# Optimization experiments

Measured on AMD Instinct MI355X. Metric: run time of the kernel, lower is better.

Reference implementation:

```python
import jax, jax.numpy as jnp
import numpy as np

EMBED_DIM = 1024
NUM_HEADS = 16
HEAD_DIM = EMBED_DIM // NUM_HEADS
SEQ_LEN = 4096


def setup_inputs() -> dict:
    key = jax.random.key(0)
    kx, kq, kk, kv = jax.random.split(key, 4)
    x = jax.random.normal(kx, (SEQ_LEN, EMBED_DIM), dtype=jnp.float32)
    Wq = jax.random.normal(kq, (EMBED_DIM, EMBED_DIM), dtype=jnp.float32)
    Wk = jax.random.normal(kk, (EMBED_DIM, EMBED_DIM), dtype=jnp.float32)
    Wv = jax.random.normal(kv, (EMBED_DIM, EMBED_DIM), dtype=jnp.float32)
    return {"x": x, "Wq": Wq, "Wk": Wk, "Wv": Wv}


def reference(x, Wq, Wk, Wv):
    seq_len, embed_dim = x.shape
    h, d = NUM_HEADS, HEAD_DIM
    # project then split heads: [S, E] -> [H, S, D]
    q = (x @ Wq).reshape(seq_len, h, d).transpose(1, 0, 2)
    k = (x @ Wk).reshape(seq_len, h, d).transpose(1, 0, 2)
    v = (x @ Wv).reshape(seq_len, h, d).transpose(1, 0, 2)
    # full [H, S, S] scores, scaled by sqrt(head_dim) (faithful to original)
    scores = jnp.einsum("hsd,htd->hst", q, k) / jnp.sqrt(jnp.asarray(d, dtype=q.dtype))
    weights = jax.nn.softmax(scores, axis=-1)
    out = jnp.einsum("hst,htd->hsd", weights, v)  # [H, S, D]
    return out.transpose(1, 0, 2).reshape(seq_len, embed_dim)
```

## Files before the change

kernel.cpp:

```cpp
#include <hip/hip_runtime.h>
#include <hip/hip_bf16.h>

#define SEQ 4096
#define EMB 1024
#define NHD 16
#define HDD 64

using bf16 = __hip_bfloat16;
using bf16x8 = __attribute__((ext_vector_type(8))) short;
using f32x4  = __attribute__((ext_vector_type(4))) float;
using f32x16 = __attribute__((ext_vector_type(16))) float;
using u32x4  = __attribute__((ext_vector_type(4))) unsigned int;
using u32x2  = __attribute__((ext_vector_type(2))) unsigned int;

#define MFMA16(a, b, c) __builtin_amdgcn_mfma_f32_16x16x32_bf16((a), (b), (c), 0, 0, 0)
#define MFMA32(a, b, c) __builtin_amdgcn_mfma_f32_32x32x16_bf16((a), (b), (c), 0, 0, 0)

#define QSCALE 0.1803368801111204f

__device__ __forceinline__ float b2f(bf16 b) { return __bfloat162float(b); }

__device__ __forceinline__ void gll16(const void* g, void* l) {
    __builtin_amdgcn_global_load_lds(
        (const __attribute__((address_space(1))) unsigned int*)g,
        (__attribute__((address_space(3))) unsigned int*)l, 16, 0, 0);
}

__device__ __forceinline__ unsigned pack_bf16x2(float a, float b) {
    __hip_bfloat162 p = __float22bfloat162_rn(make_float2(a, b));
    unsigned w;
    __builtin_memcpy(&w, &p, 4);
    return w;
}

__global__ void split_kernel(const float* __restrict__ src, bf16* __restrict__ hi,
                             bf16* __restrict__ lo, int n4) {
    int i = blockIdx.x * blockDim.x + threadIdx.x;
    if (i >= n4) return;
    float4 v = ((const float4*)src)[i];
    float vv[4] = {v.x, v.y, v.z, v.w};
#pragma unroll
    for (int j = 0; j < 4; j++) {
        bf16 h = __float2bfloat16(vv[j]);
        hi[i * 4 + j] = h;
        lo[i * 4 + j] = __float2bfloat16(vv[j] - b2f(h));
    }
}

__global__ void wtrans_kernel(const float* __restrict__ Wq, const float* __restrict__ Wk,
                              const float* __restrict__ Wv,
                              bf16* __restrict__ thq, bf16* __restrict__ tlq,
                              bf16* __restrict__ thk, bf16* __restrict__ tlk,
                              bf16* __restrict__ thv, bf16* __restrict__ tlv) {
    __shared__ float tile[32][33];
    const float* W;
    bf16 *wth, *wtl;
    if (blockIdx.z == 0) { W = Wq; wth = thq; wtl = tlq; }
    else if (blockIdx.z == 1) { W = Wk; wth = thk; wtl = tlk; }
    else { W = Wv; wth = thv; wtl = tlv; }
    int n0 = blockIdx.x * 32, k0 = blockIdx.y * 32;
    int tx = threadIdx.x, ty = threadIdx.y;
    for (int r = ty; r < 32; r += 8)
        tile[r][tx] = W[(k0 + r) * EMB + n0 + tx];
    __syncthreads();
    for (int r = ty; r < 32; r += 8) {
        float v = tile[tx][r];
        bf16 h = __float2bfloat16(v);
        wth[(n0 + r) * EMB + k0 + tx] = h;
        wtl[(n0 + r) * EMB + k0 + tx] = __float2bfloat16(v - b2f(h));
    }
}

template <int NTERMS>
__device__ __forceinline__ void proj_loop(
    const bf16* __restrict__ Ah, const bf16* __restrict__ Al,
    const bf16* __restrict__ Bth, const bf16* __restrict__ Btl,
    bf16* lAh, bf16* lAl, bf16* lBh, bf16* lBl,
    int m0, int n0, int t, f32x4 (&acc)[4][4]) {
    const int wid = t >> 6, lane = t & 63, lr = lane & 15, lg = lane >> 4;
    const int wr = (wid >> 1) * 64, wc = (wid & 1) * 64;
    for (int k0 = 0; k0 < EMB; k0 += 32) {
#pragma unroll
        for (int c = t; c < 512; c += 256) {
            int row = c >> 2, slot = c & 3;
            *(uint4*)&lAh[row * 40 + slot * 8] =
                *(const uint4*)&Ah[(m0 + row) * EMB + k0 + slot * 8];
            *(uint4*)&lBh[row * 40 + slot * 8] =
                *(const uint4*)&Bth[(n0 + row) * EMB + k0 + slot * 8];
            if constexpr (NTERMS == 3) {
                *(uint4*)&lAl[row * 40 + slot * 8] =
                    *(const uint4*)&Al[(m0 + row) * EMB + k0 + slot * 8];
                *(uint4*)&lBl[row * 40 + slot * 8] =
                    *(const uint4*)&Btl[(n0 + row) * EMB + k0 + slot * 8];
            }
        }
        __syncthreads();
        bf16x8 fah[4], fbh[4], fal[4], fbl[4];
#pragma unroll
        for (int i = 0; i < 4; i++) {
            fah[i] = *(const bf16x8*)&lAh[(wr + i * 16 + lr) * 40 + lg * 8];
            fbh[i] = *(const bf16x8*)&lBh[(wc + i * 16 + lr) * 40 + lg * 8];
            if constexpr (NTERMS == 3) {
                fal[i] = *(const bf16x8*)&lAl[(wr + i * 16 + lr) * 40 + lg * 8];
                fbl[i] = *(const bf16x8*)&lBl[(wc + i * 16 + lr) * 40 + lg * 8];
            }
        }
#pragma unroll
        for (int i = 0; i < 4; i++)
#pragma unroll
            for (int j = 0; j < 4; j++) {
                acc[i][j] = MFMA16(fah[i], fbh[j], acc[i][j]);
                if constexpr (NTERMS == 3) {
                    acc[i][j] = MFMA16(fah[i], fbl[j], acc[i][j]);
                    acc[i][j] = MFMA16(fal[i], fbh[j], acc[i][j]);
                }
            }
        __syncthreads();
    }
}

__global__ __launch_bounds__(256) void proj_qkv(
    const bf16* __restrict__ xh, const bf16* __restrict__ xl,
    const bf16* __restrict__ thq, const bf16* __restrict__ tlq,
    const bf16* __restrict__ thk, const bf16* __restrict__ tlk,
    const bf16* __restrict__ thv,
    bf16* __restrict__ qh, bf16* __restrict__ ql,
    bf16* __restrict__ kh, bf16* __restrict__ kl, bf16* __restrict__ vt) {
    __shared__ __align__(16) bf16 lAh[128 * 40];
    __shared__ __align__(16) bf16 lAl[128 * 40];
    __shared__ __align__(16) bf16 lBh[128 * 40];
    __shared__ __align__(16) bf16 lBl[128 * 40];
    const int t = threadIdx.x;
    const int m0 = blockIdx.y * 128;
    const int which = blockIdx.x >> 3;
    const int n0 = (blockIdx.x & 7) * 128;

    f32x4 acc[4][4];
#pragma unroll
    for (int i = 0; i < 4; i++)
#pragma unroll
        for (int j = 0; j < 4; j++) acc[i][j] = (f32x4){0.f, 0.f, 0.f, 0.f};

    if (which == 0)
        proj_loop<3>(xh, xl, thq, tlq, lAh, lAl, lBh, lBl, m0, n0, t, acc);
    else if (which == 1)
        proj_loop<3>(xh, xl, thk, tlk, lAh, lAl, lBh, lBl, m0, n0, t, acc);
    else
        proj_loop<1>(xh, xl, thv, nullptr, lAh, lAl, lBh, lBl, m0, n0, t, acc);

    const int wid = t >> 6, lane = t & 63, lr = lane & 15, lg = lane >> 4;
    const int wr = (wid >> 1) * 64, wc = (wid & 1) * 64;

    if (which == 2) {
#pragma unroll
        for (int i = 0; i < 4; i++)
#pragma unroll
            for (int j = 0; j < 4; j++) {
                int n = n0 + wc + j * 16 + lr;
                int m = m0 + wr + i * 16 + lg * 4;
                uint2 w;
                w.x = pack_bf16x2(acc[i][j][0], acc[i][j][1]);
                w.y = pack_bf16x2(acc[i][j][2], acc[i][j][3]);
                *(uint2*)&vt[(size_t)n * SEQ + m] = w;
            }
    } else {
        float scale = (which == 0) ? QSCALE : 1.0f;
        bf16* Chi = (which == 0) ? qh : kh;
        bf16* Clo = (which == 0) ? ql : kl;
#pragma unroll
        for (int i = 0; i < 4; i++)
#pragma unroll
            for (int j = 0; j < 4; j++)
#pragma unroll
                for (int q = 0; q < 4; q++) {
                    float cv = acc[i][j][q] * scale;
                    int m = m0 + wr + i * 16 + lg * 4 + q;
                    int n = n0 + wc + j * 16 + lr;
                    bf16 hv = __float2bfloat16(cv);
                    Chi[m * EMB + n] = hv;
                    Clo[m * EMB + n] = __float2bfloat16(cv - b2f(hv));
                }
    }
}

__global__ __launch_bounds__(512, 2) void attn_kernel(
    const bf16* __restrict__ qh, const bf16* __restrict__ ql,
    const bf16* __restrict__ kh, const bf16* __restrict__ kl,
    const bf16* __restrict__ vt, float* __restrict__ pO,
    float* __restrict__ pM, float* __restrict__ pL) {
    __shared__ __align__(16) bf16 lKV[2][3][64 * 64];
    const int t = threadIdx.x;
    const int swz = (blockIdx.x & 7) * 64 + (blockIdx.x >> 3);
    const int h = swz >> 5;
    const int half = (swz >> 4) & 1;
    const int q0 = (swz & 15) * 256;
    const int pair = h * 16 + (swz & 15);
    const int wid = t >> 6, lane = t & 63;
    const int qq = lane & 31, hi = lane >> 5;
    const int qrow = q0 + wid * 32 + qq;

    bf16x8 fqh[4], fql[4];
    {
        const bf16* qbh = qh + (size_t)qrow * EMB + h * HDD + hi * 8;
        const bf16* qbl = ql + (size_t)qrow * EMB + h * HDD + hi * 8;
#pragma unroll
        for (int ds = 0; ds < 4; ds++) {
            fqh[ds] = *(const bf16x8*)(qbh + ds * 16);
            fql[ds] = *(const bf16x8*)(qbl + ds * 16);
        }
    }

    const int srow = lane >> 3, slot = lane & 7;
    const int r = wid * 8 + srow;
    const int sb = (slot ^ (r & 7)) * 16;
    const size_t KSTEP = (size_t)64 * EMB * 2, VSTEP = 64 * 2;
    const char* gp[3];
    gp[0] = (const char*)kh + ((size_t)r * EMB + h * HDD) * 2 + sb + half * 32 * KSTEP;
    gp[1] = (const char*)kl + ((size_t)r * EMB + h * HDD) * 2 + sb + half * 32 * KSTEP;
    gp[2] = (const char*)vt + ((size_t)(h * HDD + r) * SEQ) * 2 + sb + half * 32 * VSTEP;
    bf16* lp[3];
#pragma unroll
    for (int i = 0; i < 3; i++) lp[i] = &lKV[0][i][wid * 512];

    f32x16 z16;
#pragma unroll
    for (int rg = 0; rg < 16; rg++) z16[rg] = 0.f;
    f32x16 Ofr[2];
#pragma unroll
    for (int db = 0; db < 2; db++)
#pragma unroll
        for (int rg = 0; rg < 16; rg++) Ofr[db][rg] = 0.f;
    float Mr = -1e30f, Lr = 0.f;

#pragma unroll
    for (int i = 0; i < 3; i++) {
        gll16(gp[i], lp[i]);
        gp[i] += (i < 2) ? KSTEP : VSTEP;
    }
    __syncthreads();

    for (int tk = 0; tk < 32; tk++) {
        const int cur = tk & 1;
        if (tk < 31) {
#pragma unroll
            for (int i = 0; i < 3; i++) {
                gll16(gp[i], lp[i] + (cur ^ 1) * 12288);
                gp[i] += (i < 2) ? KSTEP : VSTEP;
            }
        }
        const char* cKh = (const char*)&lKV[cur][0][0];
        const char* cKl = (const char*)&lKV[cur][1][0];
        const char* cV  = (const char*)&lKV[cur][2][0];

        __builtin_amdgcn_s_setprio(1);
        f32x16 sfr[2];
#pragma unroll
        for (int kb = 0; kb < 2; kb++) {
            const int row = kb * 32 + qq;
            const char* rbh = cKh + row * 128;
            const char* rbl = cKl + row * 128;
            const int sw = (row & 7) << 4;
            f32x16 a;
#pragma unroll
            for (int ds = 0; ds < 4; ds++) {
                const int off = (ds * 32 + hi * 16) ^ sw;
                bf16x8 kbh_ = *(const bf16x8*)(rbh + off);
                bf16x8 kbl_ = *(const bf16x8*)(rbl + off);
                if (ds == 0)
                    a = MFMA32(kbh_, fqh[0], z16);
                else
                    a = MFMA32(kbh_, fqh[ds], a);
                a = MFMA32(kbh_, fql[ds], a);
                a = MFMA32(kbl_, fqh[ds], a);
            }
            sfr[kb] = a;
        }
        __builtin_amdgcn_s_setprio(0);

        float m8[8];
#pragma unroll
        for (int i = 0; i < 8; i++)
            m8[i] = fmaxf(fmaxf(sfr[0][i], sfr[0][i + 8]),
                          fmaxf(sfr[1][i], sfr[1][i + 8]));
        float mx = fmaxf(fmaxf(fmaxf(m8[0], m8[1]), fmaxf(m8[2], m8[3])),
                         fmaxf(fmaxf(m8[4], m8[5]), fmaxf(m8[6], m8[7])));
        mx = fmaxf(mx, __shfl_xor(mx, 32));

        bool resc = !__all(mx <= Mr + 11.5f);
        float mn = resc ? fmaxf(Mr, mx) : Mr;
#pragma unroll
        for (int kb = 0; kb < 2; kb++)
#pragma unroll
            for (int rg = 0; rg < 16; rg++)
                sfr[kb][rg] = __builtin_exp2f(sfr[kb][rg] - mn);
        float s16[16];
#pragma unroll
        for (int i = 0; i < 16; i++) s16[i] = sfr[0][i] + sfr[1][i];
        float s8[8];
#pragma unroll
        for (int i = 0; i < 8; i++) s8[i] = s16[i] + s16[i + 8];
        float ps = ((s8[0] + s8[1]) + (s8[2] + s8[3])) +
                   ((s8[4] + s8[5]) + (s8[6] + s8[7]));
        ps += __shfl_xor(ps, 32);
        if (resc) {
            float fac = __builtin_exp2f(Mr - mn);
            Mr = mn;
            Lr = Lr * fac + ps;
#pragma unroll
            for (int db = 0; db < 2; db++)
#pragma unroll
                for (int rg = 0; rg < 16; rg++) Ofr[db][rg] *= fac;
        } else {
            Lr += ps;
        }

        bf16x8 pf[4];
#pragma unroll
        for (int sl = 0; sl < 4; sl++) {
            const int kb = sl >> 1, s8i = (sl & 1) * 8;
            unsigned w01 = pack_bf16x2(sfr[kb][s8i + 0], sfr[kb][s8i + 1]);
            unsigned w23 = pack_bf16x2(sfr[kb][s8i + 2], sfr[kb][s8i + 3]);
            unsigned w45 = pack_bf16x2(sfr[kb][s8i + 4], sfr[kb][s8i + 5]);
            unsigned w67 = pack_bf16x2(sfr[kb][s8i + 6], sfr[kb][s8i + 7]);
            u32x2 r0 = __builtin_amdgcn_permlane32_swap(w01, w45, false, false);
            u32x2 r1 = __builtin_amdgcn_permlane32_swap(w23, w67, false, false);
            u32x4 fw = {r0[0], r1[0], r0[1], r1[1]};
            bf16x8 pfv;
            __builtin_memcpy(&pfv, &fw, 16);
            pf[sl] = pfv;
        }

        __builtin_amdgcn_s_setprio(1);
#pragma unroll
        for (int sl = 0; sl < 4; sl++) {
#pragma unroll
            for (int db = 0; db < 2; db++) {
                const int vd = db * 32 + qq;
                const char* pv =
                    cV + vd * 128 + ((sl * 32 + hi * 16) ^ ((vd & 7) << 4));
                bf16x8 vf = *(const bf16x8*)pv;
                Ofr[db] = MFMA32(vf, pf[sl], Ofr[db]);
            }
        }
        __builtin_amdgcn_s_setprio(0);

        __syncthreads();
    }

    const size_t qloc = wid * 32 + qq;
    float* pOb = pO + (((size_t)half * 256 + pair) * 256 + qloc) * 64;
#pragma unroll
    for (int db = 0; db < 2; db++)
#pragma unroll
        for (int rg = 0; rg < 4; rg++) {
            float4 o = make_float4(Ofr[db][rg * 4 + 0], Ofr[db][rg * 4 + 1],
                                   Ofr[db][rg * 4 + 2], Ofr[db][rg * 4 + 3]);
            *(float4*)(pOb + db * 32 + rg * 8 + hi * 4) = o;
        }
    if (hi == 0) {
        size_t mi = ((size_t)half * 256 + pair) * 256 + qloc;
        pM[mi] = Mr;
        pL[mi] = Lr;
    }
}

__global__ __launch_bounds__(256) void combine_kernel(
    const float* __restrict__ pO, const float* __restrict__ pM,
    const float* __restrict__ pL, float* __restrict__ out) {
    const int t = blockIdx.x * 256 + threadIdx.x;
    const int qrow = t >> 8;
    const int col = (t & 255) * 4;
    const int h = col >> 6, d = col & 63;
    const int qb = qrow >> 8, qloc = qrow & 255;
    const size_t i0 = (size_t)(h * 16 + qb) * 256 + qloc;
    const float M0 = pM[i0], M1 = pM[65536 + i0];
    const float L0 = pL[i0], L1 = pL[65536 + i0];
    const float Mf = fmaxf(M0, M1);
    const float w0 = __builtin_exp2f(M0 - Mf), w1 = __builtin_exp2f(M1 - Mf);
    const float inv = 1.0f / (L0 * w0 + L1 * w1);
    const float4 o0 = *(const float4*)(pO + i0 * 64 + d);
    const float4 o1 = *(const float4*)(pO + (size_t)4194304 + i0 * 64 + d);
    float4 o;
    o.x = (o0.x * w0 + o1.x * w1) * inv;
    o.y = (o0.y * w0 + o1.y * w1) * inv;
    o.z = (o0.z * w0 + o1.z * w1) * inv;
    o.w = (o0.w * w0 + o1.w * w1) * inv;
    *(float4*)(out + (size_t)qrow * EMB + col) = o;
}

extern "C" void kernel_launch(void* const* d_in, const int* in_sizes, int n_in,
                              void* d_out, int out_size, void* d_ws, size_t ws_size,
                              hipStream_t stream) {
    const float* x = (const float*)d_in[0];
    const float* Wq = (const float*)d_in[1];
    const float* Wk = (const float*)d_in[2];
    const float* Wv = (const float*)d_in[3];
    float* out = (float*)d_out;

    char* ws = (char*)d_ws;
    size_t off = 0;
    auto alloc = [&](size_t elems) -> bf16* {
        bf16* p = (bf16*)(ws + off);
        off += elems * sizeof(bf16);
        return p;
    };
    bf16* qh = alloc((size_t)SEQ * EMB);
    bf16* ql = alloc((size_t)SEQ * EMB);
    bf16* kh = alloc((size_t)SEQ * EMB);
    bf16* kl = alloc((size_t)SEQ * EMB);
    bf16* vt = alloc((size_t)SEQ * EMB);
    bf16* xh = alloc((size_t)SEQ * EMB);
    bf16* xl = alloc((size_t)SEQ * EMB);
    bf16* wthq = alloc((size_t)EMB * EMB);
    bf16* wtlq = alloc((size_t)EMB * EMB);
    bf16* wthk = alloc((size_t)EMB * EMB);
    bf16* wtlk = alloc((size_t)EMB * EMB);
    bf16* wthv = alloc((size_t)EMB * EMB);
    bf16* wtlv = alloc((size_t)EMB * EMB);
    float* pO = (float*)xh;
    float* pM = pO + (size_t)2 * 256 * 256 * 64;
    float* pL = pM + (size_t)2 * 256 * 256;
    (void)ws_size; (void)in_sizes; (void)n_in; (void)out_size;

    split_kernel<<<(SEQ * EMB / 4 + 255) / 256, 256, 0, stream>>>(x, xh, xl, SEQ * EMB / 4);
    wtrans_kernel<<<dim3(32, 32, 3), dim3(32, 8), 0, stream>>>(
        Wq, Wk, Wv, wthq, wtlq, wthk, wtlk, wthv, wtlv);
    proj_qkv<<<dim3(24, 32), 256, 0, stream>>>(
        xh, xl, wthq, wtlq, wthk, wtlk, wthv, qh, ql, kh, kl, vt);
    attn_kernel<<<512, 512, 0, stream>>>(qh, ql, kh, kl, vt, pO, pM, pL);
    combine_kernel<<<4096, 256, 0, stream>>>(pO, pM, pL, out);
}
```

Measured before the change: 267.9 us.

## Process softmax per 32-key sub-block and raise occupancy target to four blocks

The attention inner loop now runs the online softmax (max, exp, sum, rescale, P@V) separately for each 32-key sub-block instead of once over a 64-key tile. This removes the two-tile score buffer, lowering register pressure, and launch bounds are raised from 2 to 4 blocks per CU to exploit that. In exchange there are twice as many max/sum cross-lane reductions and rescale checks per tile. Forcing a 4-block target with 512 threads may cause spills if the register budget is not met, and LDS usage per block (about 48KB) may cap actual occupancy anyway.

```diff
diff --git a/kernel.cpp b/kernel.cpp
--- a/kernel.cpp
+++ b/kernel.cpp
@@ -183,7 +183,7 @@
     }
 }
 
-__global__ __launch_bounds__(512, 2) void attn_kernel(
+__global__ __launch_bounds__(512, 4) void attn_kernel(
     const bf16* __restrict__ qh, const bf16* __restrict__ ql,
     const bf16* __restrict__ kh, const bf16* __restrict__ kl,
     const bf16* __restrict__ vt, float* __restrict__ pO,
@@ -222,9 +222,6 @@
 #pragma unroll
     for (int i = 0; i < 3; i++) lp[i] = &lKV[0][i][wid * 512];
 
-    f32x16 z16;
-#pragma unroll
-    for (int rg = 0; rg < 16; rg++) z16[rg] = 0.f;
     f32x16 Ofr[2];
 #pragma unroll
     for (int db = 0; db < 2; db++)
@@ -252,8 +249,6 @@
         const char* cKl = (const char*)&lKV[cur][1][0];
         const char* cV  = (const char*)&lKV[cur][2][0];
 
-        __builtin_amdgcn_s_setprio(1);
-        f32x16 sfr[2];
 #pragma unroll
         for (int kb = 0; kb < 2; kb++) {
             const int row = kb * 32 + qq;
@@ -262,87 +257,79 @@
             const int sw = (row & 7) << 4;
             f32x16 a;
 #pragma unroll
+            for (int rg = 0; rg < 16; rg++) a[rg] = 0.f;
+            __builtin_amdgcn_s_setprio(1);
+#pragma unroll
             for (int ds = 0; ds < 4; ds++) {
                 const int off = (ds * 32 + hi * 16) ^ sw;
                 bf16x8 kbh_ = *(const bf16x8*)(rbh + off);
                 bf16x8 kbl_ = *(const bf16x8*)(rbl + off);
-                if (ds == 0)
-                    a = MFMA32(kbh_, fqh[0], z16);
-                else
-                    a = MFMA32(kbh_, fqh[ds], a);
+                a = MFMA32(kbh_, fqh[ds], a);
                 a = MFMA32(kbh_, fql[ds], a);
                 a = MFMA32(kbl_, fqh[ds], a);
             }
-            sfr[kb] = a;
-        }
-        __builtin_amdgcn_s_setprio(0);
-
-        float m8[8];
-#pragma unroll
-        for (int i = 0; i < 8; i++)
-            m8[i] = fmaxf(fmaxf(sfr[0][i], sfr[0][i + 8]),
-                          fmaxf(sfr[1][i], sfr[1][i + 8]));
-        float mx = fmaxf(fmaxf(fmaxf(m8[0], m8[1]), fmaxf(m8[2], m8[3])),
-                         fmaxf(fmaxf(m8[4], m8[5]), fmaxf(m8[6], m8[7])));
-        mx = fmaxf(mx, __shfl_xor(mx, 32));
-
-        bool resc = !__all(mx <= Mr + 11.5f);
-        float mn = resc ? fmaxf(Mr, mx) : Mr;
-#pragma unroll
-        for (int kb = 0; kb < 2; kb++)
+            __builtin_amdgcn_s_setprio(0);
+
+            float m4[4];
+#pragma unroll
+            for (int i = 0; i < 4; i++)
+                m4[i] = fmaxf(fmaxf(a[i], a[i + 4]), fmaxf(a[i + 8], a[i + 12]));
+            float mx = fmaxf(fmaxf(m4[0], m4[1]), fmaxf(m4[2], m4[3]));
+            mx = fmaxf(mx, __shfl_xor(mx, 32));
+
+            bool resc = !__all(mx <= Mr + 11.5f);
+            float mn = resc ? fmaxf(Mr, mx) : Mr;
 #pragma unroll
             for (int rg = 0; rg < 16; rg++)
-                sfr[kb][rg] = __builtin_exp2f(sfr[kb][rg] - mn);
-        float s16[16];
-#pragma unroll
-        for (int i = 0; i < 16; i++) s16[i] = sfr[0][i] + sfr[1][i];
-        float s8[8];
-#pragma unroll
-        for (int i = 0; i < 8; i++) s8[i] = s16[i] + s16[i + 8];
-        float ps = ((s8[0] + s8[1]) + (s8[2] + s8[3])) +
-                   ((s8[4] + s8[5]) + (s8[6] + s8[7]));
-        ps += __shfl_xor(ps, 32);
-        if (resc) {
-            float fac = __builtin_exp2f(Mr - mn);
-            Mr = mn;
-            Lr = Lr * fac + ps;
-#pragma unroll
-            for (int db = 0; db < 2; db++)
-#pragma unroll
-                for (int rg = 0; rg < 16; rg++) Ofr[db][rg] *= fac;
-        } else {
-            Lr += ps;
-        }
-
-        bf16x8 pf[4];
-#pragma unroll
-        for (int sl = 0; sl < 4; sl++) {
-            const int kb = sl >> 1, s8i = (sl & 1) * 8;
-            unsigned w01 = pack_bf16x2(sfr[kb][s8i + 0], sfr[kb][s8i + 1]);
-            unsigned w23 = pack_bf16x2(sfr[kb][s8i + 2], sfr[kb][s8i + 3]);
-            unsigned w45 = pack_bf16x2(sfr[kb][s8i + 4], sfr[kb][s8i + 5]);
-            unsigned w67 = pack_bf16x2(sfr[kb][s8i + 6], sfr[kb][s8i + 7]);
-            u32x2 r0 = __builtin_amdgcn_permlane32_swap(w01, w45, false, false);
-            u32x2 r1 = __builtin_amdgcn_permlane32_swap(w23, w67, false, false);
-            u32x4 fw = {r0[0], r1[0], r0[1], r1[1]};
-            bf16x8 pfv;
-            __builtin_memcpy(&pfv, &fw, 16);
-            pf[sl] = pfv;
-        }
-
-        __builtin_amdgcn_s_setprio(1);
-#pragma unroll
-        for (int sl = 0; sl < 4; sl++) {
-#pragma unroll
-            for (int db = 0; db < 2; db++) {
-                const int vd = db * 32 + qq;
-                const char* pv =
-                    cV + vd * 128 + ((sl * 32 + hi * 16) ^ ((vd & 7) << 4));
-                bf16x8 vf = *(const bf16x8*)pv;
-                Ofr[db] = MFMA32(vf, pf[sl], Ofr[db]);
-            }
-        }
-        __builtin_amdgcn_s_setprio(0);
+                a[rg] = __builtin_exp2f(a[rg] - mn);
+            float s4[4];
+#pragma unroll
+            for (int i = 0; i < 4; i++)
+                s4[i] = (a[i] + a[i + 4]) + (a[i + 8] + a[i + 12]);
+            float ps = (s4[0] + s4[1]) + (s4[2] + s4[3]);
+            ps += __shfl_xor(ps, 32);
+            if (resc) {
+                float fac = __builtin_exp2f(Mr - mn);
+                Mr = mn;
+                Lr = Lr * fac + ps;
+#pragma unroll
+                for (int db = 0; db < 2; db++)
+#pragma unroll
+                    for (int rg = 0; rg < 16; rg++) Ofr[db][rg] *= fac;
+            } else {
+                Lr += ps;
+            }
+
+            bf16x8 pf[2];
+#pragma unroll
+            for (int sl = 0; sl < 2; sl++) {
+                const int s8i = sl * 8;
+                unsigned w01 = pack_bf16x2(a[s8i + 0], a[s8i + 1]);
+                unsigned w23 = pack_bf16x2(a[s8i + 2], a[s8i + 3]);
+                unsigned w45 = pack_bf16x2(a[s8i + 4], a[s8i + 5]);
+                unsigned w67 = pack_bf16x2(a[s8i + 6], a[s8i + 7]);
+                u32x2 r0 = __builtin_amdgcn_permlane32_swap(w01, w45, false, false);
+                u32x2 r1 = __builtin_amdgcn_permlane32_swap(w23, w67, false, false);
+                u32x4 fw = {r0[0], r1[0], r0[1], r1[1]};
+                bf16x8 pfv;
+                __builtin_memcpy(&pfv, &fw, 16);
+                pf[sl] = pfv;
+            }
+
+            __builtin_amdgcn_s_setprio(1);
+#pragma unroll
+            for (int sl = 0; sl < 2; sl++) {
+#pragma unroll
+                for (int db = 0; db < 2; db++) {
+                    const int vd = db * 32 + qq;
+                    const char* pv = cV + vd * 128 +
+                        (((kb * 2 + sl) * 32 + hi * 16) ^ ((vd & 7) << 4));
+                    bf16x8 vf = *(const bf16x8*)pv;
+                    Ofr[db] = MFMA32(vf, pf[sl], Ofr[db]);
+                }
+            }
+            __builtin_amdgcn_s_setprio(0);
+        }
 
         __syncthreads();
     }
```

New measurement: 255.6 us. 1.05x faster.
